# Kernel tuning notes

Measured on AMD Instinct MI355X. Metric: run time of the kernel, lower is better.

Reference implementation:

```python
import jax, jax.numpy as jnp
import numpy as np
from jax import lax

EPS = 1e-5  # BatchNorm3d default eps


def _dwconv3d(x, w, pad):
    # x: [N,C,D,H,W], w: [C,1,k,k,k] depthwise kernel
    C = w.shape[0]
    return lax.conv_general_dilated(
        x, w,
        window_strides=(1, 1, 1),
        padding=[(pad, pad)] * 3,
        dimension_numbers=('NCDHW', 'OIDHW', 'NCDHW'),
        feature_group_count=C,
    )


def _bn_relu(y, gamma, beta, mean, var):
    # Inference-mode BatchNorm3d folded into a per-channel affine, then ReLU.
    inv = gamma / jnp.sqrt(var + EPS)          # [C]
    scale = inv.reshape(1, -1, 1, 1, 1)
    bias = (beta - mean * inv).reshape(1, -1, 1, 1, 1)
    return jax.nn.relu(y * scale + bias)


def setup_inputs() -> dict:
    key = jax.random.key(0)
    ks = jax.random.split(key, 20)
    C = 32
    x = jax.random.normal(ks[0], (2, C, 64, 128, 128), dtype=jnp.float32)
    w7 = jax.random.normal(ks[1], (C, 1, 7, 7, 7), dtype=jnp.float32) * 0.05
    w3 = jax.random.normal(ks[2], (C, 1, 3, 3, 3), dtype=jnp.float32) * 0.1
    w1 = jax.random.normal(ks[3], (C, 1, 1, 1, 1), dtype=jnp.float32) * 0.3
    def bn_params(i):
        g = jax.random.normal(ks[4 + 4 * i], (C,), dtype=jnp.float32) * 0.1 + 1.0
        b = jax.random.normal(ks[5 + 4 * i], (C,), dtype=jnp.float32) * 0.1
        m = jax.random.normal(ks[6 + 4 * i], (C,), dtype=jnp.float32) * 0.1
        v = jax.random.uniform(ks[7 + 4 * i], (C,), dtype=jnp.float32) + 0.5
        return g, b, m, v
    g7, b7, m7, v7 = bn_params(0)
    g3, b3, m3, v3 = bn_params(1)
    g1, b1, m1, v1 = bn_params(2)
    return dict(x=x, w7=w7, w3=w3, w1=w1,
                g7=g7, b7=b7, m7=m7, v7=v7,
                g3=g3, b3=b3, m3=m3, v3=v3,
                g1=g1, b1=b1, m1=m1, v1=v1)


def reference(x, w7, w3, w1,
              g7, b7, m7, v7,
              g3, b3, m3, v3,
              g1, b1, m1, v1):
    # y = relu(bn7(dw7(x))) + relu(bn3(dw3(x))) + relu(bn1(dw1(x)))
    y = _bn_relu(_dwconv3d(x, w7, 3), g7, b7, m7, v7)
    y = y + _bn_relu(_dwconv3d(x, w3, 1), g3, b3, m3, v3)
    # 1x1x1 depthwise conv == per-channel scalar multiply
    y = y + _bn_relu(x * w1[:, 0, 0, 0, 0].reshape(1, -1, 1, 1, 1), g1, b1, m1, v1)
    return jax.nn.relu(x + y)
```

## Files before the change

### kernel.cpp

```cpp
#include <hip/hip_runtime.h>
#include <hip/hip_bf16.h>

#define Dd 64
#define Hh 128
#define Ww 128
#define Cc 32

#define BD 32
#define BH 16
#define BW 16
#define ZR (BD + 6)
#define HR (BH + 6)
#define NR (ZR * HR)
#define RCOLS 24
#define BLKROW 3
#define NBLK (NR * BLKROW)

#define N7WIN 14
#define N3WIN 10
#define W3BASE (49 * N7WIN)
#define ZENT   (W3BASE + 9 * N3WIN)
#define NENT   (ZENT + 1)

typedef __attribute__((ext_vector_type(8))) short short8;
typedef __attribute__((ext_vector_type(4))) float floatx4;

static __device__ __forceinline__ unsigned short f2bf(float f) {
    unsigned u = __builtin_bit_cast(unsigned, f);
    u += 0x7fffu + ((u >> 16) & 1u);
    return (unsigned short)(u >> 16);
}

static __device__ __forceinline__ unsigned pk2(float a, float b) {
    union { __hip_bfloat162 h; unsigned u; } cv;
    cv.h = __float22bfloat162_rn(make_float2(a, b));
    return cv.u;
}

__global__ __launch_bounds__(256, 3) void replk_mfma(
    const float* __restrict__ x,
    const float* __restrict__ w7, const float* __restrict__ w3, const float* __restrict__ w1,
    const float* __restrict__ g7, const float* __restrict__ b7, const float* __restrict__ m7, const float* __restrict__ v7,
    const float* __restrict__ g3, const float* __restrict__ b3, const float* __restrict__ m3, const float* __restrict__ v3,
    const float* __restrict__ g1, const float* __restrict__ b1, const float* __restrict__ m1, const float* __restrict__ v1,
    float* __restrict__ out)
{
    __shared__ __align__(16) unsigned short tile[NR * RCOLS];
    __shared__ __align__(16) unsigned short wtab[NENT * 8];

    const int tid = threadIdx.x;

    const unsigned lid = blockIdx.x;
    const unsigned nl = (lid & 7u) * 1024u + (lid >> 3);
    const int bx = nl & 127;
    const int slab = nl >> 7;
    const int c = slab & 31;
    const int nb = slab >> 5;
    const int w0 = (bx & 7) * BW;
    const int h0 = ((bx >> 3) & 7) * BH;
    const int d0 = (bx >> 6) * BD;

    const float* xc = x + (size_t)(nb * Cc + c) * (Dd * Hh * Ww);

    for (int e = tid; e < NENT; e += 256) {
        unsigned short h8[8];
#pragma unroll
        for (int j = 0; j < 8; j++) {
            float v = 0.f;
            if (e < W3BASE) {
                int pl = e / N7WIN, a = e - pl * N7WIN;
                int t = a + j - 7;
                if ((unsigned)t < 7u)
                    v = w7[c * 343 + (pl / 7) * 49 + (pl % 7) * 7 + t];
            } else if (e < ZENT) {
                int e2 = e - W3BASE;
                int p3 = e2 / N3WIN, a = e2 - p3 * N3WIN;
                int t = a + j - 7;
                if ((unsigned)t < 3u)
                    v = w3[c * 27 + (p3 / 3) * 9 + (p3 % 3) * 3 + t];
            }
            h8[j] = f2bf(v);
        }
        uint4 pk;
        pk.x = (unsigned)h8[0] | ((unsigned)h8[1] << 16);
        pk.y = (unsigned)h8[2] | ((unsigned)h8[3] << 16);
        pk.z = (unsigned)h8[4] | ((unsigned)h8[5] << 16);
        pk.w = (unsigned)h8[6] | ((unsigned)h8[7] << 16);
        *(uint4*)&wtab[e * 8] = pk;
    }

#pragma unroll
    for (int it = 0; it < 10; it++) {
        int s = tid + it * 256;
        if (s < NBLK) {
            int R = s / BLKROW, bl = s - R * BLKROW;
            int zi = R / HR, hr = R - zi * HR;
            int gz = d0 - 3 + zi, gh = h0 - 3 + hr, gw0 = w0 - 4 + bl * 8;
            float v[8];
#pragma unroll
            for (int j = 0; j < 8; j++) v[j] = 0.f;
            if ((unsigned)gz < (unsigned)Dd && (unsigned)gh < (unsigned)Hh) {
                const float* src = xc + ((size_t)gz * Hh + gh) * Ww + gw0;
                if (gw0 >= 0 && gw0 + 8 <= Ww) {
                    float4 a = *(const float4*)src;
                    float4 b = *(const float4*)(src + 4);
                    v[0] = a.x; v[1] = a.y; v[2] = a.z; v[3] = a.w;
                    v[4] = b.x; v[5] = b.y; v[6] = b.z; v[7] = b.w;
                } else {
#pragma unroll
                    for (int j = 0; j < 8; j++) {
                        int gw = gw0 + j;
                        if ((unsigned)gw < (unsigned)Ww) v[j] = src[j];
                    }
                }
            }
            uint4 pk;
            pk.x = pk2(v[0], v[1]);
            pk.y = pk2(v[2], v[3]);
            pk.z = pk2(v[4], v[5]);
            pk.w = pk2(v[6], v[7]);
            *(uint4*)&tile[R * RCOLS + bl * 8] = pk;
        }
    }

    const float eps = 1e-5f;
    const float iv7 = g7[c] / sqrtf(v7[c] + eps);
    const float bb7 = b7[c] - m7[c] * iv7;
    const float iv3 = g3[c] / sqrtf(v3[c] + eps);
    const float bb3 = b3[c] - m3[c] * iv3;
    const float iv1 = g1[c] / sqrtf(v1[c] + eps);
    const float bb1 = b1[c] - m1[c] * iv1;
    const float s1 = w1[c] * iv1;

    __syncthreads();

    const int lane = tid & 63;
    const int wave = tid >> 6;
    const int q = lane & 15;
    const int p = lane >> 4;
    const int cg = (p == 3) ? 0 : p;
    const int zbase = wave * 8;

    const int astart = 8 * p - q + 15;
    const bool ok7 = (unsigned)(astart - 9) < (unsigned)N7WIN;
    const bool ok3 = (unsigned)(astart - 11) < (unsigned)N3WIN;
    const int mul7 = ok7 ? N7WIN : 0;
    const int off7 = ok7 ? (astart - 9) : ZENT;
    const int mul3 = ok3 ? N3WIN : 0;
    const int off3 = ok3 ? (W3BASE + astart - 11) : ZENT;
    const short8* wf = (const short8*)wtab;

    floatx4 acc7[8], acc3[8];
#pragma unroll
    for (int i = 0; i < 8; i++) { acc7[i] = (floatx4)0.f; acc3[i] = (floatx4)0.f; }

#pragma unroll 1
    for (int kh = 0; kh < 7; kh++) {
        short8 A7k[7];
#pragma unroll
        for (int kd = 0; kd < 7; kd++)
            A7k[kd] = wf[(kd * 7 + kh) * mul7 + off7];

        const bool has3 = (kh >= 2) && (kh < 5);
        short8 A3k[3] = {};
        if (has3) {
            const int kh3 = kh - 2;
#pragma unroll
            for (int kd3 = 0; kd3 < 3; kd3++)
                A3k[kd3] = wf[(kd3 * 3 + kh3) * mul3 + off3];
        }

#pragma unroll
        for (int zi = 0; zi < 14; zi++) {
            const int R = (zbase + zi) * HR + q + kh;
            short8 B = *(const short8*)&tile[R * RCOLS + cg * 8];
            __builtin_amdgcn_s_setprio(1);
#pragma unroll
            for (int kd = 6; kd >= 0; kd--) {
                const int dd = zi - kd;
                if (dd >= 0 && dd < 8)
                    acc7[dd] = __builtin_amdgcn_mfma_f32_16x16x32_bf16(
                        A7k[kd], B, acc7[dd], 0, 0, 0);
            }
            if (has3) {
#pragma unroll
                for (int kd3 = 2; kd3 >= 0; kd3--) {
                    const int dd = zi - 2 - kd3;
                    if (dd >= 0 && dd < 8)
                        acc3[dd] = __builtin_amdgcn_mfma_f32_16x16x32_bf16(
                            A3k[kd3], B, acc3[dd], 0, 0, 0);
                }
            }
            __builtin_amdgcn_s_setprio(0);
        }
    }

#pragma unroll
    for (int dd = 0; dd < 8; dd++) {
        int d = d0 + zbase + dd;
        const int R = (zbase + dd + 3) * HR + (q + 3);
        uint2 u = *(const uint2*)&tile[R * RCOLS + 4 * p + 4];
        float xr[4];
        xr[0] = __builtin_bit_cast(float, u.x << 16);
        xr[1] = __builtin_bit_cast(float, u.x & 0xffff0000u);
        xr[2] = __builtin_bit_cast(float, u.y << 16);
        xr[3] = __builtin_bit_cast(float, u.y & 0xffff0000u);

        size_t off = ((size_t)(nb * Cc + c) * Dd + d) * (Hh * Ww)
                   + (size_t)(h0 + q) * Ww + w0 + p * 4;
        float o[4];
#pragma unroll
        for (int r = 0; r < 4; r++) {
            float y7 = fmaxf(fmaf(acc7[dd][r], iv7, bb7), 0.f);
            float y3 = fmaxf(fmaf(acc3[dd][r], iv3, bb3), 0.f);
            float y1 = fmaxf(fmaf(xr[r], s1, bb1), 0.f);
            o[r] = fmaxf(xr[r] + y7 + y3 + y1, 0.f);
        }
        *(float4*)(out + off) = make_float4(o[0], o[1], o[2], o[3]);
    }
}

extern "C" void kernel_launch(void* const* d_in, const int* in_sizes, int n_in,
                              void* d_out, int out_size, void* d_ws, size_t ws_size,
                              hipStream_t stream) {
    const float* x  = (const float*)d_in[0];
    const float* w7 = (const float*)d_in[1];
    const float* w3 = (const float*)d_in[2];
    const float* w1 = (const float*)d_in[3];
    const float* g7 = (const float*)d_in[4];
    const float* b7 = (const float*)d_in[5];
    const float* m7 = (const float*)d_in[6];
    const float* v7 = (const float*)d_in[7];
    const float* g3 = (const float*)d_in[8];
    const float* b3 = (const float*)d_in[9];
    const float* m3 = (const float*)d_in[10];
    const float* v3 = (const float*)d_in[11];
    const float* g1 = (const float*)d_in[12];
    const float* b1 = (const float*)d_in[13];
    const float* m1 = (const float*)d_in[14];
    const float* v1 = (const float*)d_in[15];
    float* out = (float*)d_out;

    dim3 grid(8192);
    dim3 block(256);
    hipLaunchKernelGGL(replk_mfma, grid, block, 0, stream,
                       x, w7, w3, w1, g7, b7, m7, v7, g3, b3, m3, v3,
                       g1, b1, m1, v1, out);
}
```

Measured before the change: 279.8 us.

## Remap MFMA K-dimension to pack two kh taps and two depth outputs per instruction

Restructures the MFMA formulation so that the 32-wide K dimension covers two kh taps times 16 w-window entries, and the 16-wide M dimension covers two output depth slices times eight w positions. The previous layout wasted a quarter of K on zero padding (p==3 lanes). The new layout runs four kh-group iterations instead of seven, with two B loads per z-row. It adds more weight-table register loads, a different accumulator layout, and a more complex output mapping, which risks register pressure at the 3-waves-per-SIMD launch bound.

```diff
diff --git a/kernel.cpp b/kernel.cpp
--- a/kernel.cpp
+++ b/kernel.cpp
@@ -138,57 +138,82 @@
     const int wave = tid >> 6;
     const int q = lane & 15;
     const int p = lane >> 4;
-    const int cg = (p == 3) ? 0 : p;
+    const int khp = p >> 1;
+    const int kb  = p & 1;
+    const int ddl = q >> 3;
+    const int mwq = q & 7;
     const int zbase = wave * 8;
 
-    const int astart = 8 * p - q + 15;
-    const bool ok7 = (unsigned)(astart - 9) < (unsigned)N7WIN;
-    const bool ok3 = (unsigned)(astart - 11) < (unsigned)N3WIN;
-    const int mul7 = ok7 ? N7WIN : 0;
-    const int off7 = ok7 ? (astart - 9) : ZENT;
-    const int mul3 = ok3 ? N3WIN : 0;
-    const int off3 = ok3 ? (W3BASE + astart - 11) : ZENT;
+    const int a7 = 8 * kb - mwq + 6;
+    const int a3 = a7 - 2;
     const short8* wf = (const short8*)wtab;
 
-    floatx4 acc7[8], acc3[8];
-#pragma unroll
-    for (int i = 0; i < 8; i++) { acc7[i] = (floatx4)0.f; acc3[i] = (floatx4)0.f; }
+    floatx4 acc7[4][2], acc3[4][2];
+#pragma unroll
+    for (int i = 0; i < 4; i++)
+#pragma unroll
+        for (int wh = 0; wh < 2; wh++) { acc7[i][wh] = (floatx4)0.f; acc3[i][wh] = (floatx4)0.f; }
 
 #pragma unroll 1
-    for (int kh = 0; kh < 7; kh++) {
-        short8 A7k[7];
-#pragma unroll
-        for (int kd = 0; kd < 7; kd++)
-            A7k[kd] = wf[(kd * 7 + kh) * mul7 + off7];
-
-        const bool has3 = (kh >= 2) && (kh < 5);
-        short8 A3k[3] = {};
+    for (int khg = 0; khg < 4; khg++) {
+        const int kh = 2 * khg + khp;
+        const bool ok7 = ((unsigned)a7 < 14u) && (kh <= 6);
+        const int cb7 = ok7 ? (kh * 14 + a7 - ddl * 98) : (int)ZENT;
+        const int st7 = ok7 ? 98 : 0;
+        short8 A7g[8];
+#pragma unroll
+        for (int rz = 0; rz < 8; rz++) {
+            int idx = cb7 + rz * st7;
+            if (rz == 0) idx = (ddl == 0 && ok7) ? idx : (int)ZENT;
+            if (rz == 7) idx = (ddl == 1 && ok7) ? idx : (int)ZENT;
+            A7g[rz] = wf[idx];
+        }
+
+        const bool has3 = (khg == 1) || (khg == 2);
+        short8 A3g[4] = {};
         if (has3) {
-            const int kh3 = kh - 2;
-#pragma unroll
-            for (int kd3 = 0; kd3 < 3; kd3++)
-                A3k[kd3] = wf[(kd3 * 3 + kh3) * mul3 + off3];
-        }
+            const int kh3 = 2 * (khg - 1) + khp;
+            const bool ok3 = ((unsigned)a3 < 10u) && (kh3 <= 2);
+            const int cb3 = ok3 ? (W3BASE + kh3 * 10 + a3 - ddl * 30) : (int)ZENT;
+            const int st3 = ok3 ? 30 : 0;
+#pragma unroll
+            for (int rz = 0; rz < 4; rz++) {
+                int idx = cb3 + rz * st3;
+                if (rz == 0) idx = (ddl == 0 && ok3) ? idx : (int)ZENT;
+                if (rz == 3) idx = (ddl == 1 && ok3) ? idx : (int)ZENT;
+                A3g[rz] = wf[idx];
+            }
+        }
+
+        const int rowadd = (khg == 3) ? 6 : (2 * khg + khp);
 
 #pragma unroll
         for (int zi = 0; zi < 14; zi++) {
-            const int R = (zbase + zi) * HR + q + kh;
-            short8 B = *(const short8*)&tile[R * RCOLS + cg * 8];
+            const int R = (zbase + zi) * HR + q + rowadd;
+            const unsigned short* bp = &tile[R * RCOLS + 8 * kb];
+            short8 B0 = *(const short8*)bp;
+            short8 B1 = *(const short8*)(bp + 8);
             __builtin_amdgcn_s_setprio(1);
 #pragma unroll
-            for (int kd = 6; kd >= 0; kd--) {
-                const int dd = zi - kd;
-                if (dd >= 0 && dd < 8)
-                    acc7[dd] = __builtin_amdgcn_mfma_f32_16x16x32_bf16(
-                        A7k[kd], B, acc7[dd], 0, 0, 0);
+            for (int ddg = 0; ddg < 4; ddg++) {
+                const int rz = zi - 2 * ddg;
+                if (rz >= 0 && rz < 8) {
+                    acc7[ddg][0] = __builtin_amdgcn_mfma_f32_16x16x32_bf16(
+                        A7g[rz], B0, acc7[ddg][0], 0, 0, 0);
+                    acc7[ddg][1] = __builtin_amdgcn_mfma_f32_16x16x32_bf16(
+                        A7g[rz], B1, acc7[ddg][1], 0, 0, 0);
+                }
             }
             if (has3) {
 #pragma unroll
-                for (int kd3 = 2; kd3 >= 0; kd3--) {
-                    const int dd = zi - 2 - kd3;
-                    if (dd >= 0 && dd < 8)
-                        acc3[dd] = __builtin_amdgcn_mfma_f32_16x16x32_bf16(
-                            A3k[kd3], B, acc3[dd], 0, 0, 0);
+                for (int ddg = 0; ddg < 4; ddg++) {
+                    const int rz3 = zi - 2 - 2 * ddg;
+                    if (rz3 >= 0 && rz3 < 4) {
+                        acc3[ddg][0] = __builtin_amdgcn_mfma_f32_16x16x32_bf16(
+                            A3g[rz3], B0, acc3[ddg][0], 0, 0, 0);
+                        acc3[ddg][1] = __builtin_amdgcn_mfma_f32_16x16x32_bf16(
+                            A3g[rz3], B1, acc3[ddg][1], 0, 0, 0);
+                    }
                 }
             }
             __builtin_amdgcn_s_setprio(0);
@@ -196,27 +221,30 @@
     }
 
 #pragma unroll
-    for (int dd = 0; dd < 8; dd++) {
-        int d = d0 + zbase + dd;
-        const int R = (zbase + dd + 3) * HR + (q + 3);
-        uint2 u = *(const uint2*)&tile[R * RCOLS + 4 * p + 4];
-        float xr[4];
-        xr[0] = __builtin_bit_cast(float, u.x << 16);
-        xr[1] = __builtin_bit_cast(float, u.x & 0xffff0000u);
-        xr[2] = __builtin_bit_cast(float, u.y << 16);
-        xr[3] = __builtin_bit_cast(float, u.y & 0xffff0000u);
-
-        size_t off = ((size_t)(nb * Cc + c) * Dd + d) * (Hh * Ww)
-                   + (size_t)(h0 + q) * Ww + w0 + p * 4;
-        float o[4];
-#pragma unroll
-        for (int r = 0; r < 4; r++) {
-            float y7 = fmaxf(fmaf(acc7[dd][r], iv7, bb7), 0.f);
-            float y3 = fmaxf(fmaf(acc3[dd][r], iv3, bb3), 0.f);
-            float y1 = fmaxf(fmaf(xr[r], s1, bb1), 0.f);
-            o[r] = fmaxf(xr[r] + y7 + y3 + y1, 0.f);
-        }
-        *(float4*)(out + off) = make_float4(o[0], o[1], o[2], o[3]);
+    for (int ddg = 0; ddg < 4; ddg++) {
+#pragma unroll
+        for (int wh = 0; wh < 2; wh++) {
+            const int d = d0 + zbase + 2 * ddg + khp;
+            const int Rr = (zbase + 2 * ddg + khp + 3) * HR + (q + 3);
+            uint2 u = *(const uint2*)&tile[Rr * RCOLS + 8 * wh + 4 * kb + 4];
+            float xr[4];
+            xr[0] = __builtin_bit_cast(float, u.x << 16);
+            xr[1] = __builtin_bit_cast(float, u.x & 0xffff0000u);
+            xr[2] = __builtin_bit_cast(float, u.y << 16);
+            xr[3] = __builtin_bit_cast(float, u.y & 0xffff0000u);
+
+            size_t off = ((size_t)(nb * Cc + c) * Dd + d) * (Hh * Ww)
+                       + (size_t)(h0 + q) * Ww + w0 + 8 * wh + 4 * kb;
+            float o[4];
+#pragma unroll
+            for (int r = 0; r < 4; r++) {
+                float y7 = fmaxf(fmaf(acc7[ddg][wh][r], iv7, bb7), 0.f);
+                float y3 = fmaxf(fmaf(acc3[ddg][wh][r], iv3, bb3), 0.f);
+                float y1 = fmaxf(fmaf(xr[r], s1, bb1), 0.f);
+                o[r] = fmaxf(xr[r] + y7 + y3 + y1, 0.f);
+            }
+            *(float4*)(out + off) = make_float4(o[0], o[1], o[2], o[3]);
+        }
     }
 }
 
```

After: 262.1 us. -6.3%, faster.
